# Performance work log

Hardware: AMD Instinct MI355X
Metric: run time of the kernel (lower is better)

## Reference

```python
import jax, jax.numpy as jnp
import numpy as np
from jax import lax

K = 3       # kernel_size
G = 2       # group
STRIDE = 2
BN_EPS = 1e-5


def setup_inputs() -> dict:
    key = jax.random.key(0)
    k1, k2, k3, k4, k5, k6 = jax.random.split(key, 6)
    n, c, h, w = 16, 64, 128, 128
    gk2 = G * K * K
    x = jax.random.normal(k1, (n, c, h, w), dtype=jnp.float32)
    # kaiming_normal_(fan_out) std = sqrt(2 / (out_ch * k * k))
    std = float(np.sqrt(2.0 / (gk2 * K * K)))
    conv_w = jax.random.normal(k2, (gk2, c, K, K), dtype=jnp.float32) * std
    bn_gamma = jax.random.uniform(k3, (gk2,), dtype=jnp.float32, minval=0.5, maxval=1.5)
    bn_beta = jax.random.normal(k4, (gk2,), dtype=jnp.float32) * 0.1
    bn_mean = jax.random.normal(k5, (gk2,), dtype=jnp.float32) * 0.1
    bn_var = jax.random.uniform(k6, (gk2,), dtype=jnp.float32, minval=0.5, maxval=1.5)
    return {"x": x, "conv_w": conv_w, "bn_gamma": bn_gamma, "bn_beta": bn_beta,
            "bn_mean": bn_mean, "bn_var": bn_var}


def _pasa(x, conv_w, bn_gamma, bn_beta, bn_mean, bn_var):
    n, c, h, w = x.shape
    p = K // 2
    xp = jnp.pad(x, ((0, 0), (0, 0), (p, p), (p, p)), mode="reflect")
    # attention logits: conv over padded input, 'VALID' -> same h, w
    sigma = lax.conv_general_dilated(
        xp, conv_w, window_strides=(1, 1), padding="VALID",
        dimension_numbers=("NCHW", "OIHW", "NCHW"))
    # BatchNorm (inference) folded into scale/shift
    inv = bn_gamma * lax.rsqrt(bn_var + BN_EPS)
    sigma = sigma * inv[None, :, None, None] + (bn_beta - bn_mean * inv)[None, :, None, None]
    # softmax over the full g*k*k channel dim (as in the original Softmax(dim=1))
    sigma = jax.nn.softmax(sigma, axis=1)            # [n, g*k*k, h, w]
    sigma = sigma.reshape(n, G, K * K, h, w)
    # im2col: gather k*k shifted views of the padded input -> [n, c, k*k, h, w]
    patches = jnp.stack(
        [xp[:, :, i:i + h, j:j + w] for i in range(K) for j in range(K)], axis=2)
    patches = patches.reshape(n, G, c // G, K * K, h, w)
    # softmax-weighted aggregation over the kernel window
    out = jnp.einsum("ngckhw,ngkhw->ngchw", patches, sigma).reshape(n, c, h, w)
    return out[:, :, ::STRIDE, ::STRIDE]


def reference(x, conv_w, bn_gamma, bn_beta, bn_mean, bn_var):
    return _pasa(x, conv_w, bn_gamma, bn_beta, bn_mean, bn_var)
```

## Files before the change

### kernel.cpp

```cpp
#include <hip/hip_runtime.h>

#define N_  16
#define C_  64
#define H_  128
#define W_  128
#define HO_ 64
#define WO_ 64
#define CO_ 18
#define NSP 8
#define CPS (C_/NSP)

__global__ __launch_bounds__(512, 8)
void pasa_fused2(const float* __restrict__ x,
                 const float* __restrict__ cw,
                 const float* __restrict__ gamma,
                 const float* __restrict__ beta,
                 const float* __restrict__ mean,
                 const float* __restrict__ var,
                 float* __restrict__ out)
{
    __shared__ float part[NSP][CO_][WO_];

    const int tid = threadIdx.x;
    const int wo  = tid & 63;
    const int sp  = tid >> 6;
    const int ho  = blockIdx.x;
    const int n   = blockIdx.y;

    int r0 = 2*ho - 1; if (r0 < 0) r0 = 1;
    const int r1 = 2*ho, r2 = 2*ho + 1;
    const int c1 = 2*wo, c2 = c1 + 1;
    int c0 = c1 - 1; if (c0 < 0) c0 = 1;
    (void)c2;

    const float* __restrict__ xn = x + (size_t)n * (C_*H_*W_);

    float sig[CO_];
#pragma unroll
    for (int o = 0; o < CO_; ++o) sig[o] = 0.f;

#pragma unroll 2
    for (int j = 0; j < CPS; ++j) {
        const int c = __builtin_amdgcn_readfirstlane(sp * CPS + j);
        const float* __restrict__ xc = xn + c * (H_*W_);
        const float  w0  = xc[r0*W_ + c0];
        const float2 w12 = *(const float2*)(xc + r0*W_ + c1);
        const float  w3  = xc[r1*W_ + c0];
        const float2 w45 = *(const float2*)(xc + r1*W_ + c1);
        const float  w6  = xc[r2*W_ + c0];
        const float2 w78 = *(const float2*)(xc + r2*W_ + c1);
        const float* __restrict__ wc = cw + c * 9;
#pragma unroll
        for (int o = 0; o < CO_; ++o) {
            const float* __restrict__ q = wc + o * 576;
            float a = sig[o];
            a = fmaf(w0,    q[0], a);
            a = fmaf(w12.x, q[1], a);
            a = fmaf(w12.y, q[2], a);
            a = fmaf(w3,    q[3], a);
            a = fmaf(w45.x, q[4], a);
            a = fmaf(w45.y, q[5], a);
            a = fmaf(w6,    q[6], a);
            a = fmaf(w78.x, q[7], a);
            a = fmaf(w78.y, q[8], a);
            sig[o] = a;
        }
    }

#pragma unroll
    for (int o = 0; o < CO_; ++o) part[sp][o][wo] = sig[o];
    __syncthreads();
    if (sp < 4) {
#pragma unroll
        for (int o = 0; o < CO_; ++o) part[sp][o][wo] += part[sp+4][o][wo];
    }
    __syncthreads();
    if (sp < 2) {
#pragma unroll
        for (int o = 0; o < CO_; ++o) part[sp][o][wo] += part[sp+2][o][wo];
    }
    __syncthreads();
    if (sp == 0) {
#pragma unroll
        for (int o = 0; o < CO_; ++o) part[0][o][wo] += part[1][o][wo];
    }
    __syncthreads();

    float mx = -3.4e38f;
#pragma unroll
    for (int o = 0; o < CO_; ++o) {
        const float inv = gamma[o] * rsqrtf(var[o] + 1e-5f);
        sig[o] = part[0][o][wo] * inv + (beta[o] - mean[o] * inv);
        mx = fmaxf(mx, sig[o]);
    }
    float sum = 0.f;
#pragma unroll
    for (int o = 0; o < CO_; ++o) { sig[o] = __expf(sig[o] - mx); sum += sig[o]; }
    const float rs = 1.f / sum;

    const int g = sp >> 2;
    float p[9];
    if (g == 0) {
#pragma unroll
        for (int k = 0; k < 9; ++k) p[k] = sig[k] * rs;
    } else {
#pragma unroll
        for (int k = 0; k < 9; ++k) p[k] = sig[9 + k] * rs;
    }

#pragma unroll 2
    for (int j = 0; j < CPS; ++j) {
        const int c = __builtin_amdgcn_readfirstlane(sp * CPS + j);
        const float* __restrict__ xc = xn + c * (H_*W_);
        float acc = xc[r0*W_ + c0] * p[0];
        const float2 a12 = *(const float2*)(xc + r0*W_ + c1);
        acc = fmaf(a12.x, p[1], acc);
        acc = fmaf(a12.y, p[2], acc);
        acc = fmaf(xc[r1*W_ + c0], p[3], acc);
        const float2 a45 = *(const float2*)(xc + r1*W_ + c1);
        acc = fmaf(a45.x, p[4], acc);
        acc = fmaf(a45.y, p[5], acc);
        acc = fmaf(xc[r2*W_ + c0], p[6], acc);
        const float2 a78 = *(const float2*)(xc + r2*W_ + c1);
        acc = fmaf(a78.x, p[7], acc);
        acc = fmaf(a78.y, p[8], acc);
        out[(((size_t)n*C_ + c)*HO_ + ho)*WO_ + wo] = acc;
    }
}

extern "C" void kernel_launch(void* const* d_in, const int* in_sizes, int n_in,
                              void* d_out, int out_size, void* d_ws, size_t ws_size,
                              hipStream_t stream) {
    const float* x     = (const float*)d_in[0];
    const float* cw    = (const float*)d_in[1];
    const float* gamma = (const float*)d_in[2];
    const float* beta  = (const float*)d_in[3];
    const float* mean  = (const float*)d_in[4];
    const float* var   = (const float*)d_in[5];
    float* out = (float*)d_out;

    dim3 grid(HO_, N_);
    pasa_fused2<<<grid, 512, 0, stream>>>(x, cw, gamma, beta, mean, var, out);
}
```

Measured before the change: 49.45 us.

## Prefold BN into transposed conv weights and restructure main kernel memory access

Adds a prep kernel that folds the BatchNorm scale into the conv weights, transposes them to channel-major order, and precomputes the shift, so the main kernel reads contiguous weights and skips the BN math. The main kernel also swizzles the block-to-row mapping, stores shared-memory partials as [wo][co] with float2 accesses, fully unrolls the channel loops, and drops one readfirstlane. The cost is an extra kernel launch, plus higher register pressure from the full unroll now that the occupancy hint is removed from launch_bounds.

```diff
diff --git a/kernel.cpp b/kernel.cpp
--- a/kernel.cpp
+++ b/kernel.cpp
@@ -9,98 +9,130 @@
 #define CO_ 18
 #define NSP 8
 #define CPS (C_/NSP)
+#define WSZ (C_*CO_*9)
 
-__global__ __launch_bounds__(512, 8)
-void pasa_fused2(const float* __restrict__ x,
-                 const float* __restrict__ cw,
-                 const float* __restrict__ gamma,
-                 const float* __restrict__ beta,
-                 const float* __restrict__ mean,
-                 const float* __restrict__ var,
-                 float* __restrict__ out)
+__global__ void pasa_prep(const float* __restrict__ cw,
+                          const float* __restrict__ gamma,
+                          const float* __restrict__ beta,
+                          const float* __restrict__ mean,
+                          const float* __restrict__ var,
+                          float* __restrict__ ws)
 {
-    __shared__ float part[NSP][CO_][WO_];
+    const int i = blockIdx.x * 256 + threadIdx.x;
+    if (i < WSZ) {
+        const int k = i % 9;
+        const int o = (i / 9) % CO_;
+        const int c = i / (9 * CO_);
+        const float inv = gamma[o] * rsqrtf(var[o] + 1e-5f);
+        ws[c * (CO_*9) + o * 9 + k] = cw[o * (C_*9) + c * 9 + k] * inv;
+    }
+    if (i < CO_) {
+        const float inv = gamma[i] * rsqrtf(var[i] + 1e-5f);
+        ws[WSZ + i] = beta[i] - mean[i] * inv;
+    }
+}
+
+__global__ __launch_bounds__(512)
+void pasa_main(const float* __restrict__ x,
+               const float* __restrict__ wt,
+               float* __restrict__ out)
+{
+    __shared__ float part[NSP][WO_][CO_];
 
     const int tid = threadIdx.x;
     const int wo  = tid & 63;
     const int sp  = tid >> 6;
-    const int ho  = blockIdx.x;
+    const int bx  = blockIdx.x;
+    const int ho  = ((bx & 7) << 3) | (bx >> 3);
     const int n   = blockIdx.y;
 
     int r0 = 2*ho - 1; if (r0 < 0) r0 = 1;
     const int r1 = 2*ho, r2 = 2*ho + 1;
-    const int c1 = 2*wo, c2 = c1 + 1;
+    const int c1 = 2*wo;
     int c0 = c1 - 1; if (c0 < 0) c0 = 1;
-    (void)c2;
 
-    const float* __restrict__ xn = x + (size_t)n * (C_*H_*W_);
+    const float* __restrict__ xn    = x  + (size_t)n * (C_*H_*W_);
+    const float* __restrict__ shift = wt + WSZ;
 
     float sig[CO_];
 #pragma unroll
     for (int o = 0; o < CO_; ++o) sig[o] = 0.f;
 
-#pragma unroll 2
+#pragma unroll
     for (int j = 0; j < CPS; ++j) {
         const int c = __builtin_amdgcn_readfirstlane(sp * CPS + j);
         const float* __restrict__ xc = xn + c * (H_*W_);
         const float  w0  = xc[r0*W_ + c0];
-        const float2 w12 = *(const float2*)(xc + r0*W_ + c1);
+        float2 t01 = *(const float2*)(xc + r0*W_ + c1);
         const float  w3  = xc[r1*W_ + c0];
-        const float2 w45 = *(const float2*)(xc + r1*W_ + c1);
+        float2 t45 = *(const float2*)(xc + r1*W_ + c1);
         const float  w6  = xc[r2*W_ + c0];
-        const float2 w78 = *(const float2*)(xc + r2*W_ + c1);
-        const float* __restrict__ wc = cw + c * 9;
+        float2 t78 = *(const float2*)(xc + r2*W_ + c1);
+        const float* __restrict__ q = wt + c * (CO_*9);
 #pragma unroll
         for (int o = 0; o < CO_; ++o) {
-            const float* __restrict__ q = wc + o * 576;
             float a = sig[o];
-            a = fmaf(w0,    q[0], a);
-            a = fmaf(w12.x, q[1], a);
-            a = fmaf(w12.y, q[2], a);
-            a = fmaf(w3,    q[3], a);
-            a = fmaf(w45.x, q[4], a);
-            a = fmaf(w45.y, q[5], a);
-            a = fmaf(w6,    q[6], a);
-            a = fmaf(w78.x, q[7], a);
-            a = fmaf(w78.y, q[8], a);
+            a = fmaf(w0,    q[o*9 + 0], a);
+            a = fmaf(t01.x, q[o*9 + 1], a);
+            a = fmaf(t01.y, q[o*9 + 2], a);
+            a = fmaf(w3,    q[o*9 + 3], a);
+            a = fmaf(t45.x, q[o*9 + 4], a);
+            a = fmaf(t45.y, q[o*9 + 5], a);
+            a = fmaf(w6,    q[o*9 + 6], a);
+            a = fmaf(t78.x, q[o*9 + 7], a);
+            a = fmaf(t78.y, q[o*9 + 8], a);
             sig[o] = a;
         }
     }
 
 #pragma unroll
-    for (int o = 0; o < CO_; ++o) part[sp][o][wo] = sig[o];
+    for (int i = 0; i < 9; ++i)
+        *(float2*)&part[sp][wo][2*i] = make_float2(sig[2*i], sig[2*i+1]);
     __syncthreads();
     if (sp < 4) {
 #pragma unroll
-        for (int o = 0; o < CO_; ++o) part[sp][o][wo] += part[sp+4][o][wo];
+        for (int i = 0; i < 9; ++i) {
+            const float2 a = *(const float2*)&part[sp+4][wo][2*i];
+            float2* d = (float2*)&part[sp][wo][2*i];
+            float2 b = *d; b.x += a.x; b.y += a.y; *d = b;
+        }
     }
     __syncthreads();
     if (sp < 2) {
 #pragma unroll
-        for (int o = 0; o < CO_; ++o) part[sp][o][wo] += part[sp+2][o][wo];
+        for (int i = 0; i < 9; ++i) {
+            const float2 a = *(const float2*)&part[sp+2][wo][2*i];
+            float2* d = (float2*)&part[sp][wo][2*i];
+            float2 b = *d; b.x += a.x; b.y += a.y; *d = b;
+        }
     }
     __syncthreads();
     if (sp == 0) {
 #pragma unroll
-        for (int o = 0; o < CO_; ++o) part[0][o][wo] += part[1][o][wo];
+        for (int i = 0; i < 9; ++i) {
+            const float2 a = *(const float2*)&part[1][wo][2*i];
+            float2* d = (float2*)&part[0][wo][2*i];
+            float2 b = *d; b.x += a.x; b.y += a.y; *d = b;
+        }
     }
     __syncthreads();
 
     float mx = -3.4e38f;
 #pragma unroll
-    for (int o = 0; o < CO_; ++o) {
-        const float inv = gamma[o] * rsqrtf(var[o] + 1e-5f);
-        sig[o] = part[0][o][wo] * inv + (beta[o] - mean[o] * inv);
-        mx = fmaxf(mx, sig[o]);
+    for (int i = 0; i < 9; ++i) {
+        const float2 a = *(const float2*)&part[0][wo][2*i];
+        sig[2*i]   = a.x + shift[2*i];
+        sig[2*i+1] = a.y + shift[2*i+1];
     }
+#pragma unroll
+    for (int o = 0; o < CO_; ++o) mx = fmaxf(mx, sig[o]);
     float sum = 0.f;
 #pragma unroll
     for (int o = 0; o < CO_; ++o) { sig[o] = __expf(sig[o] - mx); sum += sig[o]; }
     const float rs = 1.f / sum;
 
-    const int g = sp >> 2;
     float p[9];
-    if (g == 0) {
+    if ((sp >> 2) == 0) {
 #pragma unroll
         for (int k = 0; k < 9; ++k) p[k] = sig[k] * rs;
     } else {
@@ -108,9 +140,9 @@
         for (int k = 0; k < 9; ++k) p[k] = sig[9 + k] * rs;
     }
 
-#pragma unroll 2
+#pragma unroll
     for (int j = 0; j < CPS; ++j) {
-        const int c = __builtin_amdgcn_readfirstlane(sp * CPS + j);
+        const int c = sp * CPS + j;
         const float* __restrict__ xc = xn + c * (H_*W_);
         float acc = xc[r0*W_ + c0] * p[0];
         const float2 a12 = *(const float2*)(xc + r0*W_ + c1);
@@ -138,7 +170,9 @@
     const float* mean  = (const float*)d_in[4];
     const float* var   = (const float*)d_in[5];
     float* out = (float*)d_out;
+    float* ws  = (float*)d_ws;
 
+    pasa_prep<<<(WSZ + 255) / 256, 256, 0, stream>>>(cw, gamma, beta, mean, var, ws);
     dim3 grid(HO_, N_);
-    pasa_fused2<<<grid, 512, 0, stream>>>(x, cw, gamma, beta, mean, var, out);
+    pasa_main<<<grid, 512, 0, stream>>>(x, ws, out);
 }
```

New measurement: 64.08 us. 1.3x slower.
